# Optimization experiments

Hardware: AMD Instinct MI355X
Metric: run time of the kernel (lower is better)

Reference implementation:

```python
import jax, jax.numpy as jnp
import numpy as np

N = 100000
E = 800000
NFEAT = 128
NHID = 128
NCLASS = 40
THRESHOLD = 0.1
EPS = 1e-8


def setup_inputs() -> dict:
    key = jax.random.key(0)
    ks = jax.random.split(key, 12)
    x = jax.random.normal(ks[0], (N, NFEAT), dtype=jnp.float32)
    edge_index = jax.random.randint(ks[1], (2, E), 0, N, dtype=jnp.int64)
    edge_index2 = jax.random.randint(ks[2], (2, E), 0, N, dtype=jnp.int64)
    s1 = 1.0 / np.sqrt(NFEAT)
    s2 = 1.0 / np.sqrt(NHID)
    s3 = 1.0 / np.sqrt(NCLASS)
    W_gc1 = jax.random.uniform(ks[3], (NFEAT, NHID), jnp.float32, -s1, s1)
    b_gc1 = jax.random.uniform(ks[4], (NHID,), jnp.float32, -s1, s1)
    W_gc2 = jax.random.uniform(ks[5], (NHID, NCLASS), jnp.float32, -s2, s2)
    b_gc2 = jax.random.uniform(ks[6], (NCLASS,), jnp.float32, -s2, s2)
    W_att1 = jax.random.uniform(ks[7], (NCLASS, NCLASS), jnp.float32, -s3, s3)
    b_att1 = jax.random.uniform(ks[8], (NCLASS,), jnp.float32, -s3, s3)
    W_att2 = jax.random.uniform(ks[9], (NCLASS, 1), jnp.float32, -s3, s3)
    return {"x": x, "W_gc1": W_gc1, "b_gc1": b_gc1, "W_gc2": W_gc2,
            "b_gc2": b_gc2, "W_att1": W_att1, "b_att1": b_att1,
            "W_att2": W_att2, "edge_index": edge_index, "edge_index2": edge_index2}


def att_coef(feat, row, col, alive):
    # cosine similarity per edge; edges failing the threshold get weight 0
    # (exactly equivalent to removing them: contribute 0 to degree & messages).
    a = feat[row]          # [E, d]
    b = feat[col]          # [E, d]
    dot = jnp.sum(a * b, axis=-1)
    na = jnp.maximum(jnp.linalg.norm(a, axis=-1), EPS)
    nb = jnp.maximum(jnp.linalg.norm(b, axis=-1), EPS)
    sims = dot / (na * nb)
    mask = alive & (sims >= THRESHOLD)
    # original computes this under torch.no_grad()
    ew = jax.lax.stop_gradient(jnp.where(mask, sims, 0.0))
    return ew, mask


def gcn_conv(x, row, col, ew, W, b):
    # PyG GCNConv with add_self_loops=True, normalize=True on weighted adjacency
    h = x @ W                                     # [N, out]
    deg = jax.ops.segment_sum(ew, row, num_segments=N) + 1.0  # +1 self loop
    dinv = deg ** -0.5
    nw = dinv[row] * ew * dinv[col]               # [E]
    agg = jax.ops.segment_sum(h[col] * nw[:, None], row, num_segments=N)
    agg = agg + h * (dinv * dinv)[:, None]        # self-loop contribution
    return agg + b


def reference(x, W_gc1, b_gc1, W_gc2, b_gc2, W_att1, b_att1, W_att2,
              edge_index, edge_index2):
    r1, c1 = edge_index[0], edge_index[1]
    r2, c2 = edge_index2[0], edge_index2[1]
    ones = jnp.ones((E,), dtype=bool)

    ew2, m2 = att_coef(x, r2, c2, ones)
    ew1, m1 = att_coef(x, r1, c1, ones)

    x2 = jax.nn.relu(gcn_conv(x, r2, c2, ew2, W_gc1, b_gc1))
    x1 = jax.nn.relu(gcn_conv(x, r1, c1, ew1, W_gc1, b_gc1))
    # dropout is identity at eval time

    ew2b, _ = att_coef(x2, r2, c2, m2)
    ew1b, _ = att_coef(x1, r1, c1, m1)

    x2 = gcn_conv(x2, r2, c2, ew2b, W_gc2, b_gc2)
    x1 = gcn_conv(x1, r1, c1, ew1b, W_gc2, b_gc2)

    z = jnp.stack([x1, x2], axis=1)               # [N, 2, C]
    w = jnp.tanh(z @ W_att1 + b_att1) @ W_att2    # [N, 2, 1]
    beta = jax.nn.softmax(w, axis=1)
    fused = jnp.sum(beta * z, axis=1)             # [N, C]
    return jax.nn.log_softmax(fused, axis=1)
```

## Files before the change

kernel.cpp:

```cpp
#include <hip/hip_runtime.h>
#include <hip/hip_bf16.h>

#define NN 100000
#define EE 800000
#define THRV 0.1f
#define DELTA 0.008f
#define EPSV 1e-8f

#define ATOMIC_ADD_F32 unsafeAtomicAdd

__device__ inline int dot4(int a, int b, int c) {
#if __has_builtin(__builtin_amdgcn_sdot4)
    return __builtin_amdgcn_sdot4(a, b, c, false);
#else
    int s = c;
    #pragma unroll
    for (int k = 0; k < 4; k++) {
        int av = (a << (24 - 8 * k)) >> 24;
        int bv = (b << (24 - 8 * k)) >> 24;
        s += av * bv;
    }
    return s;
#endif
}

__device__ inline unsigned short f2bf(float f) {
    unsigned int u = __float_as_uint(f);
    u += 0x7fffu + ((u >> 16) & 1u);
    return (unsigned short)(u >> 16);
}

__device__ inline float bf2f(unsigned short s) {
    return __uint_as_float(((unsigned int)s) << 16);
}


__global__ __launch_bounds__(256) void normalize_k(const float* __restrict__ x,
                                                   unsigned short* __restrict__ xq,
                                                   float* __restrict__ rs,
                                                   float* __restrict__ norms_x,
                                                   float* __restrict__ degL1) {
    int node = blockIdx.x * 4 + (threadIdx.x >> 6);
    int lane = threadIdx.x & 63;
    float2 v = reinterpret_cast<const float2*>(x)[(size_t)node * 64 + lane];
    float ss = v.x * v.x + v.y * v.y;
    float am = fmaxf(fabsf(v.x), fabsf(v.y));
    #pragma unroll
    for (int off = 32; off; off >>= 1) {
        ss += __shfl_xor(ss, off);
        am = fmaxf(am, __shfl_xor(am, off));
    }
    float norm = fmaxf(sqrtf(ss), EPSV);
    am = fmaxf(am, 1e-12f);
    float qs = 127.0f / am;
    int q0 = __float2int_rn(v.x * qs);
    int q1 = __float2int_rn(v.y * qs);
    unsigned short packed = (unsigned short)((q0 & 0xff) | ((q1 & 0xff) << 8));
    xq[(size_t)node * 64 + lane] = packed;
    if (lane == 0) {
        norms_x[node] = norm;
        rs[node] = am / (127.0f * norm);
        degL1[node] = 1.0f;
        degL1[node + NN] = 1.0f;
    }
}


__global__ __launch_bounds__(256) void edge_sim1_k(
        const unsigned short* __restrict__ xq, const float* __restrict__ rs,
        const float* __restrict__ x, const float* __restrict__ norms_x,
        const int* __restrict__ r1, const int* __restrict__ c1,
        const int* __restrict__ r2, const int* __restrict__ c2,
        float* __restrict__ ews, float* __restrict__ degL1,
        int* __restrict__ cnt) {
    int tid = threadIdx.x;
    int e = blockIdx.x * 64 + (tid >> 2);
    int q = tid & 3;
    int rnode, cnode, gr;
    if (e < EE) { rnode = r1[e]; cnode = c1[e]; gr = rnode; }
    else { int ee = e - EE; rnode = r2[ee]; cnode = c2[ee]; gr = NN + rnode; }
    int role = q >> 1;
    int j = q & 1;
    int node = role ? cnode : rnode;
    const uint4* base = reinterpret_cast<const uint4*>(xq) + (size_t)node * 8 + j * 4;
    uint4 v0 = base[0];
    uint4 v1 = base[1];
    uint4 v2 = base[2];
    uint4 v3 = base[3];
    int d = 0;
    {
        uint4 p;
        p.x = (unsigned)__shfl_xor((int)v0.x, 2);
        p.y = (unsigned)__shfl_xor((int)v0.y, 2);
        p.z = (unsigned)__shfl_xor((int)v0.z, 2);
        p.w = (unsigned)__shfl_xor((int)v0.w, 2);
        d = dot4((int)v0.x, (int)p.x, d); d = dot4((int)v0.y, (int)p.y, d);
        d = dot4((int)v0.z, (int)p.z, d); d = dot4((int)v0.w, (int)p.w, d);
        p.x = (unsigned)__shfl_xor((int)v1.x, 2);
        p.y = (unsigned)__shfl_xor((int)v1.y, 2);
        p.z = (unsigned)__shfl_xor((int)v1.z, 2);
        p.w = (unsigned)__shfl_xor((int)v1.w, 2);
        d = dot4((int)v1.x, (int)p.x, d); d = dot4((int)v1.y, (int)p.y, d);
        d = dot4((int)v1.z, (int)p.z, d); d = dot4((int)v1.w, (int)p.w, d);
        p.x = (unsigned)__shfl_xor((int)v2.x, 2);
        p.y = (unsigned)__shfl_xor((int)v2.y, 2);
        p.z = (unsigned)__shfl_xor((int)v2.z, 2);
        p.w = (unsigned)__shfl_xor((int)v2.w, 2);
        d = dot4((int)v2.x, (int)p.x, d); d = dot4((int)v2.y, (int)p.y, d);
        d = dot4((int)v2.z, (int)p.z, d); d = dot4((int)v2.w, (int)p.w, d);
        p.x = (unsigned)__shfl_xor((int)v3.x, 2);
        p.y = (unsigned)__shfl_xor((int)v3.y, 2);
        p.z = (unsigned)__shfl_xor((int)v3.z, 2);
        p.w = (unsigned)__shfl_xor((int)v3.w, 2);
        d = dot4((int)v3.x, (int)p.x, d); d = dot4((int)v3.y, (int)p.y, d);
        d = dot4((int)v3.z, (int)p.z, d); d = dot4((int)v3.w, (int)p.w, d);
    }
    d += __shfl_xor(d, 1);
    float sim = (float)d * rs[rnode] * rs[cnode];
    if (fabsf(sim - THRV) <= DELTA) {
        const float4* xa = reinterpret_cast<const float4*>(x + (size_t)rnode * 128);
        const float4* xb = reinterpret_cast<const float4*>(x + (size_t)cnode * 128);
        float df = 0.f;
        #pragma unroll
        for (int t = 0; t < 8; t++) {
            float4 a = xa[q + 4 * t];
            float4 b = xb[q + 4 * t];
            df += a.x * b.x + a.y * b.y + a.z * b.z + a.w * b.w;
        }
        df += __shfl_xor(df, 1);
        df += __shfl_xor(df, 2);
        sim = df / (norms_x[rnode] * norms_x[cnode]);
    }
    float w = (sim >= THRV) ? sim : 0.0f;
    if (q == 0) {
        ews[e] = w;
        if (w != 0.0f) {
            ATOMIC_ADD_F32(&degL1[gr], w);
            atomicAdd(&cnt[gr], 1);
        }
    }
}


__global__ __launch_bounds__(512) void scan1_k(const int* __restrict__ in,
                                               int* __restrict__ out,
                                               int* __restrict__ partials, int n) {
    __shared__ int a[1024], b[1024];
    int t = threadIdx.x;
    int base = blockIdx.x * 1024;
    a[t]       = (base + t       < n) ? in[base + t]       : 0;
    a[t + 512] = (base + t + 512 < n) ? in[base + t + 512] : 0;
    __syncthreads();
    int* src = a; int* dst = b;
    for (int off = 1; off < 1024; off <<= 1) {
        #pragma unroll
        for (int q = 0; q < 2; q++) {
            int i = t + q * 512;
            int v = src[i];
            if (i >= off) v += src[i - off];
            dst[i] = v;
        }
        __syncthreads();
        int* tmp = src; src = dst; dst = tmp;
    }
    for (int q = 0; q < 2; q++) {
        int i = t + q * 512;
        if (base + i < n) out[base + i] = i ? src[i - 1] : 0;
    }
    if (t == 0) partials[blockIdx.x] = src[1023];
}

__global__ __launch_bounds__(256) void scan2_k(int* __restrict__ partials, int m) {
    __shared__ int a[256], b[256];
    int t = threadIdx.x;
    a[t] = (t < m) ? partials[t] : 0;
    __syncthreads();
    int* src = a; int* dst = b;
    for (int off = 1; off < 256; off <<= 1) {
        int v = src[t];
        if (t >= off) v += src[t - off];
        dst[t] = v;
        __syncthreads();
        int* tmp = src; src = dst; dst = tmp;
    }
    if (t < m) partials[t] = t ? src[t - 1] : 0;
}

__global__ void scan3_k(int* __restrict__ start, int* __restrict__ next,
                        const int* __restrict__ partials,
                        const int* __restrict__ cnt, int n) {
    int i = blockIdx.x * 256 + threadIdx.x;
    if (i < n) {
        int v = start[i] + partials[i >> 10];
        start[i] = v;
        next[i] = v;
        if (i == n - 1) start[n] = v + cnt[i];
    }
}


__global__ void scatter_alive_k(const int* __restrict__ r1, const int* __restrict__ c1,
                                const int* __restrict__ r2, const int* __restrict__ c2,
                                const float* __restrict__ ews,
                                const float* __restrict__ degL1,
                                int* __restrict__ next, int2* __restrict__ acw) {
    int e = blockIdx.x * 256 + threadIdx.x;
    float w = ews[e];
    if (w == 0.0f) return;
    int gr, c, sb;
    if (e < EE) { gr = r1[e]; c = c1[e]; sb = 0; }
    else        { gr = NN + r2[e - EE]; c = c2[e - EE]; sb = NN; }
    int pos = atomicAdd(&next[gr], 1);
    int2 rec;
    rec.x = c;
    rec.y = __float_as_int(w * rsqrtf(degL1[sb + c]));
    acw[pos] = rec;
}


__global__ __launch_bounds__(256) void gemm_nh_k(const float* __restrict__ A,
                                                 const float* __restrict__ W,
                                                 unsigned short* __restrict__ Cb, int n) {
    __shared__ float Ws[64 * 128];
    __shared__ float Xs[32 * 64];
    int tid = threadIdx.x;
    int row0 = blockIdx.x * 32;
    int cg = tid & 31;
    int rl = tid >> 5;
    float4 acc[4];
    #pragma unroll
    for (int i = 0; i < 4; i++) acc[i] = make_float4(0.f, 0.f, 0.f, 0.f);

    for (int kt = 0; kt < 2; kt++) {
        const float4* Wg = reinterpret_cast<const float4*>(W + kt * 64 * 128);
        float4* Ws4 = reinterpret_cast<float4*>(Ws);
        #pragma unroll
        for (int i = 0; i < 8; i++) Ws4[tid + 256 * i] = Wg[tid + 256 * i];
        float4* Xs4 = reinterpret_cast<float4*>(Xs);
        #pragma unroll
        for (int i = 0; i < 2; i++) {
            int idx = tid + 256 * i;
            int rr = idx >> 4, kq = idx & 15;
            int grow = row0 + rr; if (grow >= n) grow = n - 1;
            Xs4[idx] = reinterpret_cast<const float4*>(A + (size_t)grow * 128 + kt * 64)[kq];
        }
        __syncthreads();
        for (int k = 0; k < 64; k++) {
            float4 wv = reinterpret_cast<const float4*>(Ws + k * 128)[cg];
            #pragma unroll
            for (int r4 = 0; r4 < 4; r4++) {
                float xv = Xs[(rl + 8 * r4) * 64 + k];
                acc[r4].x += xv * wv.x; acc[r4].y += xv * wv.y;
                acc[r4].z += xv * wv.z; acc[r4].w += xv * wv.w;
            }
        }
        __syncthreads();
    }
    #pragma unroll
    for (int r4 = 0; r4 < 4; r4++) {
        int grow = row0 + rl + 8 * r4;
        if (grow < n) {
            ushort4 o;
            o.x = f2bf(acc[r4].x); o.y = f2bf(acc[r4].y);
            o.z = f2bf(acc[r4].z); o.w = f2bf(acc[r4].w);
            reinterpret_cast<ushort4*>(Cb + (size_t)grow * 128)[cg] = o;
        }
    }
}


__global__ __launch_bounds__(256) void agg128_fused_k(
        const unsigned short* __restrict__ hb, const int* __restrict__ start,
        const int2* __restrict__ acw, const float* __restrict__ degL1,
        const float* __restrict__ bias, unsigned int* __restrict__ aggb,
        unsigned short* __restrict__ xq2, float* __restrict__ rs2,
        float* __restrict__ norms_l2, float* __restrict__ degL2) {
    int gr = blockIdx.x * 4 + (threadIdx.x >> 6);
    int lane = threadIdx.x & 63;
    int rnode = (gr < NN) ? gr : gr - NN;
    int j0 = start[gr], j1 = start[gr + 1];
    float2 acc = make_float2(0.f, 0.f);
    for (int j = j0; j < j1; j++) {
        int2 rec = acw[j];
        float wv = __int_as_float(rec.y);
        unsigned int hv = reinterpret_cast<const unsigned int*>(hb)
                              [(size_t)rec.x * 64 + lane];
        acc.x += bf2f((unsigned short)(hv & 0xffff)) * wv;
        acc.y += bf2f((unsigned short)(hv >> 16)) * wv;
    }
    float dr = rsqrtf(degL1[gr]);
    unsigned int hs = reinterpret_cast<const unsigned int*>(hb)
                          [(size_t)rnode * 64 + lane];
    float hx = bf2f((unsigned short)(hs & 0xffff));
    float hy = bf2f((unsigned short)(hs >> 16));
    float2 bb = reinterpret_cast<const float2*>(bias)[lane];
    float vx = fmaxf(acc.x * dr + hx * dr * dr + bb.x, 0.0f);
    float vy = fmaxf(acc.y * dr + hy * dr * dr + bb.y, 0.0f);
    aggb[(size_t)gr * 64 + lane] =
        (unsigned int)f2bf(vx) | ((unsigned int)f2bf(vy) << 16);
    float ss = vx * vx + vy * vy;
    float am = fmaxf(vx, vy);
    #pragma unroll
    for (int off = 32; off; off >>= 1) {
        ss += __shfl_xor(ss, off);
        am = fmaxf(am, __shfl_xor(am, off));
    }
    float norm = fmaxf(sqrtf(ss), EPSV);
    am = fmaxf(am, 1e-12f);
    float qs = 127.0f / am;
    int q0 = __float2int_rn(vx * qs);
    int q1 = __float2int_rn(vy * qs);
    xq2[(size_t)gr * 64 + lane] = (unsigned short)((q0 & 0xff) | ((q1 & 0xff) << 8));
    if (lane == 0) {
        rs2[gr] = am / (127.0f * norm);
        norms_l2[gr] = norm;
        degL2[gr] = 1.0f;
    }
}


__global__ __launch_bounds__(256) void edge_sim2_k(
        const unsigned short* __restrict__ xq2, const float* __restrict__ rs2,
        const unsigned int* __restrict__ aggb, const float* __restrict__ norms_l2,
        const int* __restrict__ start, int2* __restrict__ acw,
        float* __restrict__ degL2) {
    int gr = blockIdx.x * 4 + (threadIdx.x >> 6);
    int lane = threadIdx.x & 63;
    int j0 = start[gr], j1 = start[gr + 1];
    if (j0 == j1) return;
    int set_base = (gr < NN) ? 0 : NN;
    unsigned int au = xq2[(size_t)gr * 64 + lane];
    int a0 = ((int)(au << 24)) >> 24;
    int a1 = ((int)((au << 16) & 0xff000000u)) >> 24;
    float ra = rs2[gr];
    float nr = norms_l2[gr];
    float sum = 0.f;
    for (int j = j0; j < j1; j++) {
        int2 rec = acw[j];
        int cg = set_base + rec.x;
        unsigned int bu = xq2[(size_t)cg * 64 + lane];
        int b0 = ((int)(bu << 24)) >> 24;
        int b1 = ((int)((bu << 16) & 0xff000000u)) >> 24;
        int d = a0 * b0 + a1 * b1;
        #pragma unroll
        for (int off = 32; off; off >>= 1) d += __shfl_xor(d, off);
        float sim = (float)d * ra * rs2[cg];
        if (fabsf(sim - THRV) <= DELTA) {
            unsigned int av = aggb[(size_t)gr * 64 + lane];
            unsigned int bv = aggb[(size_t)cg * 64 + lane];
            float df = bf2f((unsigned short)(av & 0xffff)) *
                       bf2f((unsigned short)(bv & 0xffff)) +
                       bf2f((unsigned short)(av >> 16)) *
                       bf2f((unsigned short)(bv >> 16));
            #pragma unroll
            for (int off = 32; off; off >>= 1) df += __shfl_xor(df, off);
            sim = df / (nr * norms_l2[cg]);
        }
        float w2 = (sim >= THRV) ? sim : 0.0f;
        if (lane == 0) acw[j].y = __float_as_int(w2);
        sum += w2;
    }
    if (lane == 0) degL2[gr] = 1.0f + sum;
}


__global__ __launch_bounds__(256) void gemm_nc_k(const unsigned short* __restrict__ Ab,
                                                 const float* __restrict__ W,
                                                 unsigned short* __restrict__ Cb, int n) {
    __shared__ float Ws[128 * 40];
    __shared__ float Xs[64 * 130];
    int tid = threadIdx.x;
    int row0 = blockIdx.x * 64;
    for (int i = tid; i < 128 * 40; i += 256) Ws[i] = W[i];
    #pragma unroll
    for (int i = 0; i < 4; i++) {
        int idx = tid + 256 * i;
        int rr = idx >> 4, kq = idx & 15;
        int grow = row0 + rr; if (grow >= n) grow = n - 1;
        uint4 v = reinterpret_cast<const uint4*>(Ab + (size_t)grow * 128)[kq];
        float* dst = &Xs[rr * 130 + kq * 8];
        dst[0] = bf2f((unsigned short)(v.x & 0xffff));
        dst[1] = bf2f((unsigned short)(v.x >> 16));
        dst[2] = bf2f((unsigned short)(v.y & 0xffff));
        dst[3] = bf2f((unsigned short)(v.y >> 16));
        dst[4] = bf2f((unsigned short)(v.z & 0xffff));
        dst[5] = bf2f((unsigned short)(v.z >> 16));
        dst[6] = bf2f((unsigned short)(v.w & 0xffff));
        dst[7] = bf2f((unsigned short)(v.w >> 16));
    }
    __syncthreads();
    int c5 = tid & 7;
    int r  = tid >> 3;
    float acc0[5] = {0, 0, 0, 0, 0}, acc1[5] = {0, 0, 0, 0, 0};
    for (int k = 0; k < 128; k++) {
        float x0 = Xs[r * 130 + k], x1 = Xs[(r + 32) * 130 + k];
        #pragma unroll
        for (int c = 0; c < 5; c++) {
            float wv = Ws[k * 40 + c5 * 5 + c];
            acc0[c] += x0 * wv; acc1[c] += x1 * wv;
        }
    }
    int g0 = row0 + r, g1 = row0 + r + 32;
    if (g0 < n) {
        for (int c = 0; c < 5; c++)
            Cb[(size_t)g0 * 64 + c5 * 5 + c] = f2bf(acc0[c]);
    }
    if (g1 < n) {
        for (int c = 0; c < 5; c++)
            Cb[(size_t)g1 * 64 + c5 * 5 + c] = f2bf(acc1[c]);
    }
}


__global__ __launch_bounds__(256) void agg40_fused_k(
        const unsigned short* __restrict__ h2b, const int* __restrict__ start,
        const int2* __restrict__ acw, const float* __restrict__ degL2,
        const float* __restrict__ bias, float* __restrict__ aggy) {
    int gr = blockIdx.x * 4 + (threadIdx.x >> 6);
    int lane = threadIdx.x & 63;
    int set_base = (gr < NN) ? 0 : NN;
    int j0 = start[gr], j1 = start[gr + 1];
    bool act = lane < 40;
    float acc = 0.f;
    for (int j = j0; j < j1; j++) {
        int2 rec = acw[j];
        float w2 = __int_as_float(rec.y);
        if (w2 == 0.0f) continue;
        int cg = set_base + rec.x;
        float nv = w2 * rsqrtf(degL2[cg]);
        float hv = act ? bf2f(h2b[(size_t)cg * 64 + lane]) : 0.f;
        acc += hv * nv;
    }
    if (act) {
        float dr = rsqrtf(degL2[gr]);
        float self = bf2f(h2b[(size_t)gr * 64 + lane]);
        aggy[(size_t)gr * 40 + lane] = acc * dr + self * dr * dr + bias[lane];
    }
}


__global__ __launch_bounds__(256) void fusion_k(const float* __restrict__ y1,
                                                const float* __restrict__ y2,
                                                const float* __restrict__ W1,
                                                const float* __restrict__ b1,
                                                const float* __restrict__ W2,
                                                float* __restrict__ out, int n) {
    __shared__ float W1s[40 * 40];
    __shared__ float b1s[40];
    __shared__ float W2s[40];
    int tid = threadIdx.x;
    for (int i = tid; i < 1600; i += 256) W1s[i] = W1[i];
    if (tid < 40) { b1s[tid] = b1[tid]; W2s[tid] = W2[tid]; }
    __syncthreads();
    int i = blockIdx.x * 256 + tid;
    if (i >= n) return;
    float z1[40], z2[40];
    const float4* y14 = reinterpret_cast<const float4*>(y1 + (size_t)i * 40);
    const float4* y24 = reinterpret_cast<const float4*>(y2 + (size_t)i * 40);
    #pragma unroll
    for (int q = 0; q < 10; q++) {
        float4 a = y14[q], b = y24[q];
        z1[4 * q] = a.x; z1[4 * q + 1] = a.y; z1[4 * q + 2] = a.z; z1[4 * q + 3] = a.w;
        z2[4 * q] = b.x; z2[4 * q + 1] = b.y; z2[4 * q + 2] = b.z; z2[4 * q + 3] = b.w;
    }
    float w1 = 0.f, w2 = 0.f;
    for (int c = 0; c < 40; c++) {
        float s1 = b1s[c], s2 = b1s[c];
        for (int j = 0; j < 40; j++) {
            float ww = W1s[j * 40 + c];
            s1 += z1[j] * ww; s2 += z2[j] * ww;
        }
        float wa = W2s[c];
        w1 += tanhf(s1) * wa; w2 += tanhf(s2) * wa;
    }
    float m = fmaxf(w1, w2);
    float e1 = expf(w1 - m), e2 = expf(w2 - m);
    float inv = 1.0f / (e1 + e2);
    float be1 = e1 * inv, be2 = e2 * inv;
    float fu[40];
    float mx = -1e30f;
    #pragma unroll
    for (int c = 0; c < 40; c++) {
        fu[c] = be1 * z1[c] + be2 * z2[c];
        mx = fmaxf(mx, fu[c]);
    }
    float se = 0.f;
    #pragma unroll
    for (int c = 0; c < 40; c++) se += expf(fu[c] - mx);
    float ls = logf(se);
    float4* o4 = reinterpret_cast<float4*>(out + (size_t)i * 40);
    #pragma unroll
    for (int q = 0; q < 10; q++) {
        float4 v;
        v.x = fu[4 * q] - mx - ls; v.y = fu[4 * q + 1] - mx - ls;
        v.z = fu[4 * q + 2] - mx - ls; v.w = fu[4 * q + 3] - mx - ls;
        o4[q] = v;
    }
}


extern "C" void kernel_launch(void* const* d_in, const int* in_sizes, int n_in,
                              void* d_out, int out_size, void* d_ws, size_t ws_size,
                              hipStream_t stream) {
    (void)in_sizes; (void)n_in; (void)out_size; (void)ws_size;
    const float* x   = (const float*)d_in[0];
    const float* Wg1 = (const float*)d_in[1];
    const float* bg1 = (const float*)d_in[2];
    const float* Wg2 = (const float*)d_in[3];
    const float* bg2 = (const float*)d_in[4];
    const float* Wa1 = (const float*)d_in[5];
    const float* ba1 = (const float*)d_in[6];
    const float* Wa2 = (const float*)d_in[7];
    const int* ei1 = (const int*)d_in[8];
    const int* ei2 = (const int*)d_in[9];
    const int *r1 = ei1, *c1 = ei1 + EE;
    const int *r2 = ei2, *c2 = ei2 + EE;
    float* out = (float*)d_out;

    float* wp = (float*)d_ws;
    float* norms_x  = wp;  wp += NN;
    float* norms_l2 = wp;  wp += 2 * NN;
    float* rs       = wp;  wp += NN;
    float* degL1    = wp;  wp += 2 * NN;
    float* degL2    = wp;  wp += 2 * NN;
    int*   cnt      = (int*)wp;  wp += 2 * NN;
    int*   start    = (int*)wp;  wp += 2 * NN + 8;
    int*   next     = (int*)wp;  wp += 2 * NN;
    int*   partials = (int*)wp;  wp += 512;
    float* ews      = wp;  wp += 2 * EE;
    int2*  acw      = (int2*)wp; wp += (size_t)2 * 2 * EE;
    unsigned short* hb  = (unsigned short*)wp; wp += (size_t)NN * 64;
    unsigned short* h2b = (unsigned short*)wp; wp += (size_t)2 * NN * 32;
    unsigned int*   aggb = (unsigned int*)wp;  wp += (size_t)2 * NN * 64;
    unsigned short* xq2 = (unsigned short*)wp; wp += (size_t)2 * NN * 32;
    unsigned short* xq = (unsigned short*)aggb;
    float* rs2  = ews;
    float* aggy = (float*)aggb;

    const int twoN = 2 * NN;
    const int twoE = 2 * EE;
    const int scan_blocks = (twoN + 1023) / 1024;

    (void)hipMemsetAsync(cnt, 0, sizeof(int) * twoN, stream);
    normalize_k<<<NN / 4, 256, 0, stream>>>(x, xq, rs, norms_x, degL1);
    edge_sim1_k<<<twoE / 64, 256, 0, stream>>>(xq, rs, x, norms_x,
                                               r1, c1, r2, c2, ews, degL1, cnt);

    scan1_k<<<scan_blocks, 512, 0, stream>>>(cnt, start, partials, twoN);
    scan2_k<<<1, 256, 0, stream>>>(partials, scan_blocks);
    scan3_k<<<(twoN + 255) / 256, 256, 0, stream>>>(start, next, partials, cnt, twoN);
    scatter_alive_k<<<twoE / 256, 256, 0, stream>>>(r1, c1, r2, c2, ews, degL1,
                                                    next, acw);

    gemm_nh_k<<<NN / 32, 256, 0, stream>>>(x, Wg1, hb, NN);
    agg128_fused_k<<<twoN / 4, 256, 0, stream>>>(hb, start, acw, degL1, bg1,
                                                 aggb, xq2, rs2, norms_l2, degL2);

    edge_sim2_k<<<twoN / 4, 256, 0, stream>>>(xq2, rs2, aggb, norms_l2,
                                              start, acw, degL2);
    gemm_nc_k<<<twoN / 64, 256, 0, stream>>>((const unsigned short*)aggb, Wg2,
                                             h2b, twoN);
    agg40_fused_k<<<twoN / 4, 256, 0, stream>>>(h2b, start, acw, degL2, bg2, aggy);

    fusion_k<<<(NN + 255) / 256, 256, 0, stream>>>(aggy, aggy + (size_t)NN * 40,
                                                   Wa1, ba1, Wa2, out, NN);
}
```

Measured before the change: 466.2 us.

## Fuse GEMM1 into edge-sim kernel, int8 hidden features, fuse agg40 with fusion head

The first-layer GEMM now runs as extra blocks of the edge-similarity kernel, and its output is quantized per row to int8 with a scale. The scale is folded into the edge weights during scatter. The cnt memset is folded into normalize_k, and edge_sim1 uses 8 threads per edge instead of 4. agg40 and the attention/log-softmax fusion are merged into one wave-per-node kernel, so the intermediate aggy buffer is no longer written and re-read. Int8 hidden features lower gather bandwidth in agg128 at the cost of more quantization error.

```diff
diff --git a/kernel.cpp b/kernel.cpp
--- a/kernel.cpp
+++ b/kernel.cpp
@@ -6,6 +6,7 @@
 #define THRV 0.1f
 #define DELTA 0.008f
 #define EPSV 1e-8f
+#define GEMMB 3125
 
 #define ATOMIC_ADD_F32 unsafeAtomicAdd
 
@@ -39,7 +40,8 @@
                                                    unsigned short* __restrict__ xq,
                                                    float* __restrict__ rs,
                                                    float* __restrict__ norms_x,
-                                                   float* __restrict__ degL1) {
+                                                   float* __restrict__ degL1,
+                                                   int* __restrict__ cnt) {
     int node = blockIdx.x * 4 + (threadIdx.x >> 6);
     int lane = threadIdx.x & 63;
     float2 v = reinterpret_cast<const float2*>(x)[(size_t)node * 64 + lane];
@@ -55,80 +57,125 @@
     float qs = 127.0f / am;
     int q0 = __float2int_rn(v.x * qs);
     int q1 = __float2int_rn(v.y * qs);
-    unsigned short packed = (unsigned short)((q0 & 0xff) | ((q1 & 0xff) << 8));
-    xq[(size_t)node * 64 + lane] = packed;
+    xq[(size_t)node * 64 + lane] = (unsigned short)((q0 & 0xff) | ((q1 & 0xff) << 8));
     if (lane == 0) {
         norms_x[node] = norm;
         rs[node] = am / (127.0f * norm);
         degL1[node] = 1.0f;
         degL1[node + NN] = 1.0f;
-    }
-}
-
-
-__global__ __launch_bounds__(256) void edge_sim1_k(
+        cnt[node] = 0;
+        cnt[node + NN] = 0;
+    }
+}
+
+
+__global__ __launch_bounds__(256) void sim1gemm_k(
         const unsigned short* __restrict__ xq, const float* __restrict__ rs,
         const float* __restrict__ x, const float* __restrict__ norms_x,
         const int* __restrict__ r1, const int* __restrict__ c1,
         const int* __restrict__ r2, const int* __restrict__ c2,
         float* __restrict__ ews, float* __restrict__ degL1,
-        int* __restrict__ cnt) {
+        int* __restrict__ cnt,
+        const float* __restrict__ W, unsigned int* __restrict__ hq,
+        float* __restrict__ hrs) {
+    __shared__ float Ws[32 * 128];
+    __shared__ float Xs[32 * 36];
     int tid = threadIdx.x;
-    int e = blockIdx.x * 64 + (tid >> 2);
-    int q = tid & 3;
+
+    if (blockIdx.x < GEMMB) {
+        int row0 = blockIdx.x * 32;
+        int cg = tid & 31;
+        int rl = tid >> 5;
+        float4 acc[4];
+        #pragma unroll
+        for (int i = 0; i < 4; i++) acc[i] = make_float4(0.f, 0.f, 0.f, 0.f);
+        for (int kt = 0; kt < 4; kt++) {
+            const float4* Wg = reinterpret_cast<const float4*>(W + kt * 32 * 128);
+            float4* Ws4 = reinterpret_cast<float4*>(Ws);
+            #pragma unroll
+            for (int i = 0; i < 4; i++) Ws4[tid + 256 * i] = Wg[tid + 256 * i];
+            int rr = tid >> 3, kq = tid & 7;
+            float4 xv4 = reinterpret_cast<const float4*>(
+                x + (size_t)(row0 + rr) * 128 + kt * 32)[kq];
+            *reinterpret_cast<float4*>(&Xs[rr * 36 + kq * 4]) = xv4;
+            __syncthreads();
+            for (int k = 0; k < 32; k++) {
+                float4 wv = reinterpret_cast<const float4*>(Ws + k * 128)[cg];
+                #pragma unroll
+                for (int r4 = 0; r4 < 4; r4++) {
+                    float xv = Xs[(rl + 8 * r4) * 36 + k];
+                    acc[r4].x += xv * wv.x; acc[r4].y += xv * wv.y;
+                    acc[r4].z += xv * wv.z; acc[r4].w += xv * wv.w;
+                }
+            }
+            __syncthreads();
+        }
+        #pragma unroll
+        for (int r4 = 0; r4 < 4; r4++) {
+            float am = fmaxf(fmaxf(fabsf(acc[r4].x), fabsf(acc[r4].y)),
+                             fmaxf(fabsf(acc[r4].z), fabsf(acc[r4].w)));
+            #pragma unroll
+            for (int off = 1; off < 32; off <<= 1) am = fmaxf(am, __shfl_xor(am, off));
+            am = fmaxf(am, 1e-20f);
+            float qs = 127.0f / am;
+            int q0 = __float2int_rn(acc[r4].x * qs);
+            int q1 = __float2int_rn(acc[r4].y * qs);
+            int q2 = __float2int_rn(acc[r4].z * qs);
+            int q3 = __float2int_rn(acc[r4].w * qs);
+            unsigned int u = (q0 & 0xff) | ((q1 & 0xff) << 8) |
+                             ((q2 & 0xff) << 16) | ((q3 & 0xff) << 24);
+            int grow = row0 + rl + 8 * r4;
+            hq[(size_t)grow * 32 + cg] = u;
+            if (cg == 0) hrs[grow] = am / 127.0f;
+        }
+        return;
+    }
+
+    int b = blockIdx.x - GEMMB;
+    int e = b * 32 + (tid >> 3);
+    int q = tid & 7;
     int rnode, cnode, gr;
     if (e < EE) { rnode = r1[e]; cnode = c1[e]; gr = rnode; }
     else { int ee = e - EE; rnode = r2[ee]; cnode = c2[ee]; gr = NN + rnode; }
-    int role = q >> 1;
-    int j = q & 1;
+    int role = q >> 2;
+    int j = q & 3;
     int node = role ? cnode : rnode;
-    const uint4* base = reinterpret_cast<const uint4*>(xq) + (size_t)node * 8 + j * 4;
+    const uint4* base = reinterpret_cast<const uint4*>(xq) + (size_t)node * 8 + j * 2;
     uint4 v0 = base[0];
     uint4 v1 = base[1];
-    uint4 v2 = base[2];
-    uint4 v3 = base[3];
-    int d = 0;
-    {
-        uint4 p;
-        p.x = (unsigned)__shfl_xor((int)v0.x, 2);
-        p.y = (unsigned)__shfl_xor((int)v0.y, 2);
-        p.z = (unsigned)__shfl_xor((int)v0.z, 2);
-        p.w = (unsigned)__shfl_xor((int)v0.w, 2);
-        d = dot4((int)v0.x, (int)p.x, d); d = dot4((int)v0.y, (int)p.y, d);
-        d = dot4((int)v0.z, (int)p.z, d); d = dot4((int)v0.w, (int)p.w, d);
-        p.x = (unsigned)__shfl_xor((int)v1.x, 2);
-        p.y = (unsigned)__shfl_xor((int)v1.y, 2);
-        p.z = (unsigned)__shfl_xor((int)v1.z, 2);
-        p.w = (unsigned)__shfl_xor((int)v1.w, 2);
-        d = dot4((int)v1.x, (int)p.x, d); d = dot4((int)v1.y, (int)p.y, d);
-        d = dot4((int)v1.z, (int)p.z, d); d = dot4((int)v1.w, (int)p.w, d);
-        p.x = (unsigned)__shfl_xor((int)v2.x, 2);
-        p.y = (unsigned)__shfl_xor((int)v2.y, 2);
-        p.z = (unsigned)__shfl_xor((int)v2.z, 2);
-        p.w = (unsigned)__shfl_xor((int)v2.w, 2);
-        d = dot4((int)v2.x, (int)p.x, d); d = dot4((int)v2.y, (int)p.y, d);
-        d = dot4((int)v2.z, (int)p.z, d); d = dot4((int)v2.w, (int)p.w, d);
-        p.x = (unsigned)__shfl_xor((int)v3.x, 2);
-        p.y = (unsigned)__shfl_xor((int)v3.y, 2);
-        p.z = (unsigned)__shfl_xor((int)v3.z, 2);
-        p.w = (unsigned)__shfl_xor((int)v3.w, 2);
-        d = dot4((int)v3.x, (int)p.x, d); d = dot4((int)v3.y, (int)p.y, d);
-        d = dot4((int)v3.z, (int)p.z, d); d = dot4((int)v3.w, (int)p.w, d);
-    }
+    uint4 p0, p1;
+    p0.x = (unsigned)__shfl_xor((int)v0.x, 4);
+    p0.y = (unsigned)__shfl_xor((int)v0.y, 4);
+    p0.z = (unsigned)__shfl_xor((int)v0.z, 4);
+    p0.w = (unsigned)__shfl_xor((int)v0.w, 4);
+    p1.x = (unsigned)__shfl_xor((int)v1.x, 4);
+    p1.y = (unsigned)__shfl_xor((int)v1.y, 4);
+    p1.z = (unsigned)__shfl_xor((int)v1.z, 4);
+    p1.w = (unsigned)__shfl_xor((int)v1.w, 4);
+    int d = dot4((int)v0.x, (int)p0.x, 0);
+    d = dot4((int)v0.y, (int)p0.y, d);
+    d = dot4((int)v0.z, (int)p0.z, d);
+    d = dot4((int)v0.w, (int)p0.w, d);
+    d = dot4((int)v1.x, (int)p1.x, d);
+    d = dot4((int)v1.y, (int)p1.y, d);
+    d = dot4((int)v1.z, (int)p1.z, d);
+    d = dot4((int)v1.w, (int)p1.w, d);
     d += __shfl_xor(d, 1);
+    d += __shfl_xor(d, 2);
     float sim = (float)d * rs[rnode] * rs[cnode];
     if (fabsf(sim - THRV) <= DELTA) {
         const float4* xa = reinterpret_cast<const float4*>(x + (size_t)rnode * 128);
         const float4* xb = reinterpret_cast<const float4*>(x + (size_t)cnode * 128);
         float df = 0.f;
         #pragma unroll
-        for (int t = 0; t < 8; t++) {
-            float4 a = xa[q + 4 * t];
-            float4 b = xb[q + 4 * t];
-            df += a.x * b.x + a.y * b.y + a.z * b.z + a.w * b.w;
+        for (int t = 0; t < 4; t++) {
+            float4 a = xa[q + 8 * t];
+            float4 bb = xb[q + 8 * t];
+            df += a.x * bb.x + a.y * bb.y + a.z * bb.z + a.w * bb.w;
         }
         df += __shfl_xor(df, 1);
         df += __shfl_xor(df, 2);
+        df += __shfl_xor(df, 4);
         sim = df / (norms_x[rnode] * norms_x[cnode]);
     }
     float w = (sim >= THRV) ? sim : 0.0f;
@@ -203,6 +250,7 @@
                                 const int* __restrict__ r2, const int* __restrict__ c2,
                                 const float* __restrict__ ews,
                                 const float* __restrict__ degL1,
+                                const float* __restrict__ hrs,
                                 int* __restrict__ next, int2* __restrict__ acw) {
     int e = blockIdx.x * 256 + threadIdx.x;
     float w = ews[e];
@@ -213,68 +261,18 @@
     int pos = atomicAdd(&next[gr], 1);
     int2 rec;
     rec.x = c;
-    rec.y = __float_as_int(w * rsqrtf(degL1[sb + c]));
+    rec.y = __float_as_int(w * rsqrtf(degL1[sb + c]) * hrs[c]);
     acw[pos] = rec;
 }
 
 
-__global__ __launch_bounds__(256) void gemm_nh_k(const float* __restrict__ A,
-                                                 const float* __restrict__ W,
-                                                 unsigned short* __restrict__ Cb, int n) {
-    __shared__ float Ws[64 * 128];
-    __shared__ float Xs[32 * 64];
-    int tid = threadIdx.x;
-    int row0 = blockIdx.x * 32;
-    int cg = tid & 31;
-    int rl = tid >> 5;
-    float4 acc[4];
-    #pragma unroll
-    for (int i = 0; i < 4; i++) acc[i] = make_float4(0.f, 0.f, 0.f, 0.f);
-
-    for (int kt = 0; kt < 2; kt++) {
-        const float4* Wg = reinterpret_cast<const float4*>(W + kt * 64 * 128);
-        float4* Ws4 = reinterpret_cast<float4*>(Ws);
-        #pragma unroll
-        for (int i = 0; i < 8; i++) Ws4[tid + 256 * i] = Wg[tid + 256 * i];
-        float4* Xs4 = reinterpret_cast<float4*>(Xs);
-        #pragma unroll
-        for (int i = 0; i < 2; i++) {
-            int idx = tid + 256 * i;
-            int rr = idx >> 4, kq = idx & 15;
-            int grow = row0 + rr; if (grow >= n) grow = n - 1;
-            Xs4[idx] = reinterpret_cast<const float4*>(A + (size_t)grow * 128 + kt * 64)[kq];
-        }
-        __syncthreads();
-        for (int k = 0; k < 64; k++) {
-            float4 wv = reinterpret_cast<const float4*>(Ws + k * 128)[cg];
-            #pragma unroll
-            for (int r4 = 0; r4 < 4; r4++) {
-                float xv = Xs[(rl + 8 * r4) * 64 + k];
-                acc[r4].x += xv * wv.x; acc[r4].y += xv * wv.y;
-                acc[r4].z += xv * wv.z; acc[r4].w += xv * wv.w;
-            }
-        }
-        __syncthreads();
-    }
-    #pragma unroll
-    for (int r4 = 0; r4 < 4; r4++) {
-        int grow = row0 + rl + 8 * r4;
-        if (grow < n) {
-            ushort4 o;
-            o.x = f2bf(acc[r4].x); o.y = f2bf(acc[r4].y);
-            o.z = f2bf(acc[r4].z); o.w = f2bf(acc[r4].w);
-            reinterpret_cast<ushort4*>(Cb + (size_t)grow * 128)[cg] = o;
-        }
-    }
-}
-
-
 __global__ __launch_bounds__(256) void agg128_fused_k(
-        const unsigned short* __restrict__ hb, const int* __restrict__ start,
-        const int2* __restrict__ acw, const float* __restrict__ degL1,
-        const float* __restrict__ bias, unsigned int* __restrict__ aggb,
-        unsigned short* __restrict__ xq2, float* __restrict__ rs2,
-        float* __restrict__ norms_l2, float* __restrict__ degL2) {
+        const unsigned short* __restrict__ hq16, const float* __restrict__ hrs,
+        const int* __restrict__ start, const int2* __restrict__ acw,
+        const float* __restrict__ degL1, const float* __restrict__ bias,
+        unsigned int* __restrict__ aggb, unsigned short* __restrict__ xq2,
+        float* __restrict__ rs2, float* __restrict__ norms_l2,
+        float* __restrict__ degL2) {
     int gr = blockIdx.x * 4 + (threadIdx.x >> 6);
     int lane = threadIdx.x & 63;
     int rnode = (gr < NN) ? gr : gr - NN;
@@ -283,16 +281,15 @@
     for (int j = j0; j < j1; j++) {
         int2 rec = acw[j];
         float wv = __int_as_float(rec.y);
-        unsigned int hv = reinterpret_cast<const unsigned int*>(hb)
-                              [(size_t)rec.x * 64 + lane];
-        acc.x += bf2f((unsigned short)(hv & 0xffff)) * wv;
-        acc.y += bf2f((unsigned short)(hv >> 16)) * wv;
+        unsigned short hv = hq16[(size_t)rec.x * 64 + lane];
+        acc.x += (float)(char)(hv & 0xff) * wv;
+        acc.y += (float)(char)(hv >> 8) * wv;
     }
     float dr = rsqrtf(degL1[gr]);
-    unsigned int hs = reinterpret_cast<const unsigned int*>(hb)
-                          [(size_t)rnode * 64 + lane];
-    float hx = bf2f((unsigned short)(hs & 0xffff));
-    float hy = bf2f((unsigned short)(hs >> 16));
+    float hr = hrs[rnode];
+    unsigned short hs = hq16[(size_t)rnode * 64 + lane];
+    float hx = (float)(char)(hs & 0xff) * hr;
+    float hy = (float)(char)(hs >> 8) * hr;
     float2 bb = reinterpret_cast<const float2*>(bias)[lane];
     float vx = fmaxf(acc.x * dr + hx * dr * dr + bb.x, 0.0f);
     float vy = fmaxf(acc.y * dr + hy * dr * dr + bb.y, 0.0f);
@@ -412,39 +409,12 @@
 }
 
 
-__global__ __launch_bounds__(256) void agg40_fused_k(
+__global__ __launch_bounds__(256) void agg40_fusion_k(
         const unsigned short* __restrict__ h2b, const int* __restrict__ start,
         const int2* __restrict__ acw, const float* __restrict__ degL2,
-        const float* __restrict__ bias, float* __restrict__ aggy) {
-    int gr = blockIdx.x * 4 + (threadIdx.x >> 6);
-    int lane = threadIdx.x & 63;
-    int set_base = (gr < NN) ? 0 : NN;
-    int j0 = start[gr], j1 = start[gr + 1];
-    bool act = lane < 40;
-    float acc = 0.f;
-    for (int j = j0; j < j1; j++) {
-        int2 rec = acw[j];
-        float w2 = __int_as_float(rec.y);
-        if (w2 == 0.0f) continue;
-        int cg = set_base + rec.x;
-        float nv = w2 * rsqrtf(degL2[cg]);
-        float hv = act ? bf2f(h2b[(size_t)cg * 64 + lane]) : 0.f;
-        acc += hv * nv;
-    }
-    if (act) {
-        float dr = rsqrtf(degL2[gr]);
-        float self = bf2f(h2b[(size_t)gr * 64 + lane]);
-        aggy[(size_t)gr * 40 + lane] = acc * dr + self * dr * dr + bias[lane];
-    }
-}
-
-
-__global__ __launch_bounds__(256) void fusion_k(const float* __restrict__ y1,
-                                                const float* __restrict__ y2,
-                                                const float* __restrict__ W1,
-                                                const float* __restrict__ b1,
-                                                const float* __restrict__ W2,
-                                                float* __restrict__ out, int n) {
+        const float* __restrict__ bias,
+        const float* __restrict__ W1, const float* __restrict__ b1,
+        const float* __restrict__ W2, float* __restrict__ out) {
     __shared__ float W1s[40 * 40];
     __shared__ float b1s[40];
     __shared__ float W2s[40];
@@ -452,50 +422,55 @@
     for (int i = tid; i < 1600; i += 256) W1s[i] = W1[i];
     if (tid < 40) { b1s[tid] = b1[tid]; W2s[tid] = W2[tid]; }
     __syncthreads();
-    int i = blockIdx.x * 256 + tid;
-    if (i >= n) return;
-    float z1[40], z2[40];
-    const float4* y14 = reinterpret_cast<const float4*>(y1 + (size_t)i * 40);
-    const float4* y24 = reinterpret_cast<const float4*>(y2 + (size_t)i * 40);
-    #pragma unroll
-    for (int q = 0; q < 10; q++) {
-        float4 a = y14[q], b = y24[q];
-        z1[4 * q] = a.x; z1[4 * q + 1] = a.y; z1[4 * q + 2] = a.z; z1[4 * q + 3] = a.w;
-        z2[4 * q] = b.x; z2[4 * q + 1] = b.y; z2[4 * q + 2] = b.z; z2[4 * q + 3] = b.w;
-    }
-    float w1 = 0.f, w2 = 0.f;
-    for (int c = 0; c < 40; c++) {
-        float s1 = b1s[c], s2 = b1s[c];
+    int node = blockIdx.x * 4 + (tid >> 6);
+    int lane = tid & 63;
+    bool act = lane < 40;
+    float z[2];
+    #pragma unroll
+    for (int s = 0; s < 2; s++) {
+        int gr = node + s * NN;
+        int sb = s * NN;
+        int j0 = start[gr], j1 = start[gr + 1];
+        float acc = 0.f;
+        for (int j = j0; j < j1; j++) {
+            int2 rec = acw[j];
+            float w2 = __int_as_float(rec.y);
+            if (w2 == 0.0f) continue;
+            int cg = sb + rec.x;
+            float nv = w2 * rsqrtf(degL2[cg]);
+            float hv = act ? bf2f(h2b[(size_t)cg * 64 + lane]) : 0.f;
+            acc += hv * nv;
+        }
+        float dr = rsqrtf(degL2[gr]);
+        float self = act ? bf2f(h2b[(size_t)gr * 64 + lane]) : 0.f;
+        float bv = act ? bias[lane] : 0.f;
+        z[s] = acc * dr + self * dr * dr + bv;
+    }
+    float wsc[2];
+    #pragma unroll
+    for (int s = 0; s < 2; s++) {
+        float sc = act ? b1s[lane] : 0.f;
         for (int j = 0; j < 40; j++) {
-            float ww = W1s[j * 40 + c];
-            s1 += z1[j] * ww; s2 += z2[j] * ww;
-        }
-        float wa = W2s[c];
-        w1 += tanhf(s1) * wa; w2 += tanhf(s2) * wa;
-    }
-    float m = fmaxf(w1, w2);
-    float e1 = expf(w1 - m), e2 = expf(w2 - m);
+            float zj = __shfl(z[s], j);
+            if (act) sc += zj * W1s[j * 40 + lane];
+        }
+        float t = act ? tanhf(sc) * W2s[lane] : 0.f;
+        #pragma unroll
+        for (int off = 1; off < 64; off <<= 1) t += __shfl_xor(t, off);
+        wsc[s] = t;
+    }
+    float m = fmaxf(wsc[0], wsc[1]);
+    float e1 = expf(wsc[0] - m), e2 = expf(wsc[1] - m);
     float inv = 1.0f / (e1 + e2);
-    float be1 = e1 * inv, be2 = e2 * inv;
-    float fu[40];
-    float mx = -1e30f;
-    #pragma unroll
-    for (int c = 0; c < 40; c++) {
-        fu[c] = be1 * z1[c] + be2 * z2[c];
-        mx = fmaxf(mx, fu[c]);
-    }
-    float se = 0.f;
-    #pragma unroll
-    for (int c = 0; c < 40; c++) se += expf(fu[c] - mx);
-    float ls = logf(se);
-    float4* o4 = reinterpret_cast<float4*>(out + (size_t)i * 40);
-    #pragma unroll
-    for (int q = 0; q < 10; q++) {
-        float4 v;
-        v.x = fu[4 * q] - mx - ls; v.y = fu[4 * q + 1] - mx - ls;
-        v.z = fu[4 * q + 2] - mx - ls; v.w = fu[4 * q + 3] - mx - ls;
-        o4[q] = v;
-    }
+    float fu = (e1 * inv) * z[0] + (e2 * inv) * z[1];
+    float mx = act ? fu : -1e30f;
+    #pragma unroll
+    for (int off = 1; off < 64; off <<= 1) mx = fmaxf(mx, __shfl_xor(mx, off));
+    float ex = act ? expf(fu - mx) : 0.f;
+    #pragma unroll
+    for (int off = 1; off < 64; off <<= 1) ex += __shfl_xor(ex, off);
+    float ls = logf(ex);
+    if (act) out[(size_t)node * 40 + lane] = fu - mx - ls;
 }
 
 
@@ -523,45 +498,42 @@
     float* rs       = wp;  wp += NN;
     float* degL1    = wp;  wp += 2 * NN;
     float* degL2    = wp;  wp += 2 * NN;
+    float* hrs      = wp;  wp += NN;
     int*   cnt      = (int*)wp;  wp += 2 * NN;
     int*   start    = (int*)wp;  wp += 2 * NN + 8;
     int*   next     = (int*)wp;  wp += 2 * NN;
     int*   partials = (int*)wp;  wp += 512;
     float* ews      = wp;  wp += 2 * EE;
     int2*  acw      = (int2*)wp; wp += (size_t)2 * 2 * EE;
-    unsigned short* hb  = (unsigned short*)wp; wp += (size_t)NN * 64;
+    unsigned int* hq = (unsigned int*)wp; wp += (size_t)NN * 32;
     unsigned short* h2b = (unsigned short*)wp; wp += (size_t)2 * NN * 32;
     unsigned int*   aggb = (unsigned int*)wp;  wp += (size_t)2 * NN * 64;
     unsigned short* xq2 = (unsigned short*)wp; wp += (size_t)2 * NN * 32;
     unsigned short* xq = (unsigned short*)aggb;
-    float* rs2  = ews;
-    float* aggy = (float*)aggb;
+    float* rs2 = ews;
 
     const int twoN = 2 * NN;
     const int twoE = 2 * EE;
     const int scan_blocks = (twoN + 1023) / 1024;
 
-    (void)hipMemsetAsync(cnt, 0, sizeof(int) * twoN, stream);
-    normalize_k<<<NN / 4, 256, 0, stream>>>(x, xq, rs, norms_x, degL1);
-    edge_sim1_k<<<twoE / 64, 256, 0, stream>>>(xq, rs, x, norms_x,
-                                               r1, c1, r2, c2, ews, degL1, cnt);
+    normalize_k<<<NN / 4, 256, 0, stream>>>(x, xq, rs, norms_x, degL1, cnt);
+    sim1gemm_k<<<GEMMB + twoE / 32, 256, 0, stream>>>(
+        xq, rs, x, norms_x, r1, c1, r2, c2, ews, degL1, cnt, Wg1, hq, hrs);
 
     scan1_k<<<scan_blocks, 512, 0, stream>>>(cnt, start, partials, twoN);
     scan2_k<<<1, 256, 0, stream>>>(partials, scan_blocks);
     scan3_k<<<(twoN + 255) / 256, 256, 0, stream>>>(start, next, partials, cnt, twoN);
-    scatter_alive_k<<<twoE / 256, 256, 0, stream>>>(r1, c1, r2, c2, ews, degL1,
+    scatter_alive_k<<<twoE / 256, 256, 0, stream>>>(r1, c1, r2, c2, ews, degL1, hrs,
                                                     next, acw);
 
-    gemm_nh_k<<<NN / 32, 256, 0, stream>>>(x, Wg1, hb, NN);
-    agg128_fused_k<<<twoN / 4, 256, 0, stream>>>(hb, start, acw, degL1, bg1,
+    agg128_fused_k<<<twoN / 4, 256, 0, stream>>>((const unsigned short*)hq, hrs,
+                                                 start, acw, degL1, bg1,
                                                  aggb, xq2, rs2, norms_l2, degL2);
 
     edge_sim2_k<<<twoN / 4, 256, 0, stream>>>(xq2, rs2, aggb, norms_l2,
                                               start, acw, degL2);
     gemm_nc_k<<<twoN / 64, 256, 0, stream>>>((const unsigned short*)aggb, Wg2,
                                              h2b, twoN);
-    agg40_fused_k<<<twoN / 4, 256, 0, stream>>>(h2b, start, acw, degL2, bg2, aggy);
-
-    fusion_k<<<(NN + 255) / 256, 256, 0, stream>>>(aggy, aggy + (size_t)NN * 40,
-                                                   Wa1, ba1, Wa2, out, NN);
-}
+    agg40_fusion_k<<<NN / 4, 256, 0, stream>>>(h2b, start, acw, degL2, bg2,
+                                               Wa1, ba1, Wa2, out);
+}
```

Result: slower. 510.0 us (+9.4%).
